# Kernel tuning notes

Hardware: AMD Instinct MI355X
Metric: run time of the kernel (lower is better)

The kernel has to match this reference:

```python
import jax, jax.numpy as jnp
import numpy as np

NUM_HEADS = 12


def setup_inputs() -> dict:
    key = jax.random.key(0)
    k0, k1, k2 = jax.random.split(key, 3)
    B, S, D = 2, 2048, 1536
    scale = 1.0 / np.sqrt(D)
    return {
        "hidden_states": jax.random.normal(k0, (B, S, D), dtype=jnp.float32),
        "W_fc": jax.random.normal(k1, (D, D), dtype=jnp.float32) * scale,
        "b_fc": jnp.zeros((D,), dtype=jnp.float32),
        "W_proj": jax.random.normal(k2, (D, D), dtype=jnp.float32) * scale,
        "b_proj": jnp.zeros((D,), dtype=jnp.float32),
    }


def reference(hidden_states, W_fc, b_fc, W_proj, b_proj):
    B, S, D = hidden_states.shape
    H = NUM_HEADS
    hd = D // H
    # value_states: [B, H, S, hd] (key_states == value_states in the original)
    v = (hidden_states @ W_fc.T + b_fc).reshape(B, S, H, hd).transpose(0, 2, 1, 3)
    # Uniform-weight causal sliding-window attention, window_h = 2^(h+1)-1.
    i = jnp.arange(S)[:, None]          # query pos
    j = jnp.arange(S)[None, :]          # key pos
    w = (2 ** jnp.arange(1, H + 1, dtype=jnp.int32) - 1)[:, None, None]  # [H,1,1]
    mask = (j <= i) & (j >= i - w + 1)                                    # [H,S,S]
    valid_len = jnp.minimum(i + 1, w).astype(v.dtype)                     # [H,S,1]
    attn = jnp.where(mask, 1.0 / valid_len, 0.0)                          # [H,S,S]
    # [H,S,S] x [B,H,S,hd] -> [B,S,H,hd] -> [B,S,D]
    out = jnp.einsum("hqk,bhkd->bqhd", attn, v).reshape(B, S, D)
    attn_weights = jnp.broadcast_to(attn[None], (B, H, S, S))
    return out @ W_proj.T + b_proj, attn_weights
```

## Files before the change

### kernel.cpp

```cpp
#include <hip/hip_runtime.h>
#include <hip/hip_bf16.h>

#define S_LEN   2048
#define DMODEL  1536
#define NBATCH  2
#define NHEADS  12
#define MROWS   (NBATCH * S_LEN)
#define NCHUNK  64
#define CHUNK   32

#define NGEMM_BLK  384
#define AW_BLK     3072
#define AW_TOTAL4  25165824u
#define AW_HALF4   12582912u

typedef unsigned short u16;
typedef __attribute__((ext_vector_type(8))) short bf16x8;
typedef __attribute__((ext_vector_type(4))) float f32x4;

__device__ __forceinline__ u16 f2bf(float x) {
  unsigned u = __float_as_uint(x);
  u += 0x7fffu + ((u >> 16) & 1u);
  return (u16)(u >> 16);
}
__device__ __forceinline__ float bf2f(u16 x) {
  return __uint_as_float(((unsigned)x) << 16);
}

#define N4_HID  1572864
#define N4_W    589824
__global__ void cvt_all(const float4* __restrict__ h, const float4* __restrict__ wf,
                        const float4* __restrict__ wp, ushort4* __restrict__ ho,
                        ushort4* __restrict__ wfo, ushort4* __restrict__ wpo) {
  int t = blockIdx.x * blockDim.x + threadIdx.x;
  const float4* src;
  ushort4* dst;
  int idx;
  if (t < N4_HID)            { src = h;  dst = ho;  idx = t; }
  else if (t < N4_HID + N4_W){ src = wf; dst = wfo; idx = t - N4_HID; }
  else                       { src = wp; dst = wpo; idx = t - N4_HID - N4_W; }
  float4 f = src[idx];
  ushort4 o;
  o.x = f2bf(f.x); o.y = f2bf(f.y); o.z = f2bf(f.z); o.w = f2bf(f.w);
  dst[idx] = o;
}

__device__ __forceinline__ void gld_lds16(u16* lds, const u16* g) {
  __builtin_amdgcn_global_load_lds(
      (const __attribute__((address_space(1))) unsigned int*)g,
      (__attribute__((address_space(3))) unsigned int*)lds, 16, 0, 0);
}

template <bool WITH_CSUM, typename CT>
__global__ __launch_bounds__(256)
void gemm_aw(const u16* __restrict__ A, const u16* __restrict__ B,
             const float* __restrict__ bias, CT* __restrict__ C,
             float* __restrict__ cs, f32x4* __restrict__ aw,
             unsigned aw0, unsigned awcnt, int Ndim, int Kdim) {
  if ((int)blockIdx.x >= NGEMM_BLK) {
    const unsigned stride = (gridDim.x - NGEMM_BLK) * 256u;
    const unsigned end = aw0 + awcnt;
    unsigned t = aw0 + (blockIdx.x - NGEMM_BLK) * 256u + threadIdx.x;
    for (; t < end; t += stride) {
      int j0 = (int)(t & 511u) << 2;
      int i  = (int)(t >> 9) & (S_LEN - 1);
      int bh = (int)(t >> 20);
      int h  = bh >= NHEADS ? bh - NHEADS : bh;
      int w  = (2 << h) - 1;
      int len = min(i + 1, w);
      float inv = 1.0f / (float)len;
      int lo = i - w + 1;
      f32x4 r;
      r.x = (j0     <= i && j0     >= lo) ? inv : 0.f;
      r.y = (j0 + 1 <= i && j0 + 1 >= lo) ? inv : 0.f;
      r.z = (j0 + 2 <= i && j0 + 2 >= lo) ? inv : 0.f;
      r.w = (j0 + 3 <= i && j0 + 3 >= lo) ? inv : 0.f;
      __builtin_nontemporal_store(r, &aw[t]);
    }
    return;
  }

  __shared__ __align__(16) u16 As[128 * 32];
  __shared__ __align__(16) u16 Bs[128 * 32];
  __shared__ float colpart[4][128];

  const int tid  = threadIdx.x;
  const int wave = tid >> 6;
  const int lane = tid & 63;
  const int l15  = lane & 15;
  const int quad = lane >> 4;
  const int bm = (blockIdx.x / (DMODEL / 128)) * 128;
  const int bn = (blockIdx.x % (DMODEL / 128)) * 128;
  const int wm = (wave >> 1) * 64;
  const int wn = (wave & 1) * 64;

  f32x4 acc[4][4] = {};

  const int srow = wave * 32 + (lane >> 2);
  const int skk  = (lane & 3) * 8;
  const u16* gA = A + (size_t)(bm + srow) * Kdim + skk;
  const u16* gB = B + (size_t)(bn + srow) * Kdim + skk;
  u16* lA = &As[(wave * 32) * 32];
  u16* lB = &Bs[(wave * 32) * 32];
  const size_t rstep16 = (size_t)16 * Kdim;

  for (int k0 = 0; k0 < Kdim; k0 += 32) {
    gld_lds16(lA,           gA + k0);
    gld_lds16(lA + 16 * 32, gA + k0 + rstep16);
    gld_lds16(lB,           gB + k0);
    gld_lds16(lB + 16 * 32, gB + k0 + rstep16);
    __syncthreads();

    bf16x8 af[4], bfr[4];
#pragma unroll
    for (int i = 0; i < 4; ++i)
      af[i] = *(const bf16x8*)&As[(wm + i * 16 + l15) * 32 + quad * 8];
#pragma unroll
    for (int j = 0; j < 4; ++j)
      bfr[j] = *(const bf16x8*)&Bs[(wn + j * 16 + l15) * 32 + quad * 8];
#pragma unroll
    for (int i = 0; i < 4; ++i)
#pragma unroll
      for (int j = 0; j < 4; ++j)
        acc[i][j] = __builtin_amdgcn_mfma_f32_16x16x32_bf16(af[i], bfr[j], acc[i][j], 0, 0, 0);
    __syncthreads();
  }

  const int r0 = quad * 4;
#pragma unroll
  for (int j = 0; j < 4; ++j) {
    const int col = bn + wn + j * 16 + l15;
    const float bj = bias[col];
    float sA = 0.f, sB = 0.f;
#pragma unroll
    for (int i = 0; i < 4; ++i) {
      const int row = bm + wm + i * 16 + r0;
#pragma unroll
      for (int r = 0; r < 4; ++r) {
        float cv = acc[i][j][r] + bj;
        if constexpr (sizeof(CT) == 2)
          C[(size_t)(row + r) * Ndim + col] = (CT)f2bf(cv);
        else
          C[(size_t)(row + r) * Ndim + col] = (CT)cv;
        if (WITH_CSUM) { if (i < 2) sA += cv; else sB += cv; }
      }
    }
    if (WITH_CSUM) {
      sA += __shfl_xor(sA, 16); sA += __shfl_xor(sA, 32);
      sB += __shfl_xor(sB, 16); sB += __shfl_xor(sB, 32);
      if (quad == 0) {
        colpart[(wm >> 5) | 0][wn + j * 16 + l15] = sA;
        colpart[(wm >> 5) | 1][wn + j * 16 + l15] = sB;
      }
    }
  }
  if (WITH_CSUM) {
    __syncthreads();
    if (tid < 128) {
      const int b  = bm >> 11;
      const int c0 = (bm & 2047) >> 5;
#pragma unroll
      for (int g = 0; g < 4; ++g)
        cs[((size_t)b * NCHUNK + c0 + g) * DMODEL + bn + tid] = colpart[g][tid];
    }
  }
}

__global__ void chunk_prefix(const float* __restrict__ cs, float* __restrict__ E) {
  int t = blockIdx.x * blockDim.x + threadIdx.x;
  int d = t % DMODEL;
  int c = (t / DMODEL) % NCHUNK;
  int b = t / (DMODEL * NCHUNK);
  const float* p = cs + (size_t)b * NCHUNK * DMODEL + d;
  float s = 0.f;
  for (int cc = 0; cc < c; ++cc) s += p[(size_t)cc * DMODEL];
  E[t] = s;
}

__global__ void winavg_strip(const u16* __restrict__ v, const float* __restrict__ E,
                             u16* __restrict__ A2) {
  int t = blockIdx.x * blockDim.x + threadIdx.x;
  int d = t % DMODEL;
  int s = (t / DMODEL) & 255;
  int b = t / (DMODEL * 256);
  const int h = d >> 7;
  const int w = (2 << h) - 1;
  const u16* vb  = v + (size_t)b * S_LEN * DMODEL + d;
  const float* Eb = E + (size_t)b * NCHUNK * DMODEL + d;

  const int i0 = s * 8;
  float lead = Eb[(size_t)(i0 >> 5) * DMODEL];
  for (int r = i0 & ~31; r < i0; ++r)
    lead += bf2f(vb[(size_t)r * DMODEL]);

  float trail = 0.f;
  if (i0 + 7 >= w) {
    const int jf = max(i0, w) - w;
    if (jf > 0) {
      const int ct = (jf - 1) >> 5;
      trail = Eb[(size_t)ct * DMODEL];
      for (int r = ct * 32; r < jf; ++r)
        trail += bf2f(vb[(size_t)r * DMODEL]);
    }
  }

  u16* out = A2 + ((size_t)(b * S_LEN + i0)) * DMODEL + d;
#pragma unroll
  for (int rr = 0; rr < 8; ++rr) {
    const int i = i0 + rr;
    lead += bf2f(vb[(size_t)i * DMODEL]);
    float o;
    if (i < w) {
      o = lead / (float)(i + 1);
    } else {
      trail += bf2f(vb[(size_t)(i - w) * DMODEL]);
      o = (lead - trail) / (float)w;
    }
    out[(size_t)rr * DMODEL] = f2bf(o);
  }
}

extern "C" void kernel_launch(void* const* d_in, const int* in_sizes, int n_in,
                              void* d_out, int out_size, void* d_ws, size_t ws_size,
                              hipStream_t stream) {
  const float* hidden = (const float*)d_in[0];
  const float* W_fc   = (const float*)d_in[1];
  const float* b_fc   = (const float*)d_in[2];
  const float* W_proj = (const float*)d_in[3];
  const float* b_proj = (const float*)d_in[4];
  float* outp = (float*)d_out;
  f32x4* aw = (f32x4*)(outp + (size_t)MROWS * DMODEL);

  char* ws = (char*)d_ws;
  u16*   A16   = (u16*)(ws);
  u16*   Wfc16 = (u16*)(ws + 12582912);
  u16*   Wpj16 = (u16*)(ws + 17301504);
  u16*   v16   = (u16*)(ws + 22020096);
  float* csums = (float*)(ws + 34603008);
  float* Epre  = (float*)(ws + 35389440);

  cvt_all<<<10752, 256, 0, stream>>>((const float4*)hidden, (const float4*)W_fc,
                                     (const float4*)W_proj, (ushort4*)A16,
                                     (ushort4*)Wfc16, (ushort4*)Wpj16);

  gemm_aw<true, u16><<<NGEMM_BLK + AW_BLK, 256, 0, stream>>>(
      A16, Wfc16, b_fc, v16, csums, aw, 0u, AW_HALF4, DMODEL, DMODEL);

  chunk_prefix<<<(NBATCH * NCHUNK * DMODEL) / 256, 256, 0, stream>>>(csums, Epre);

  winavg_strip<<<(NBATCH * (S_LEN / 8) * DMODEL) / 256, 256, 0, stream>>>(v16, Epre, A16);

  gemm_aw<false, float><<<NGEMM_BLK + AW_BLK, 256, 0, stream>>>(
      A16, Wpj16, b_proj, outp, nullptr, aw, AW_HALF4, AW_HALF4, DMODEL, DMODEL);
}
```

Baseline: 541.1 us.

## Fuse chunk prefix into window-average kernel and rebalance attn-weight writes across launches

Removes the separate chunk_prefix launch. The window-average kernel now computes its lead and trail prefix sums directly from the chunk sums with an in-register loop. Extra blocks are added to that kernel so it writes a slice of the attention-weight tensor, and the split of that output across the three launches is rebalanced. The final GEMM output is written with nontemporal stores. Each thread now does an O(chunks) loop, but one launch and one intermediate buffer round trip go away.

```diff
diff --git a/kernel.cpp b/kernel.cpp
--- a/kernel.cpp
+++ b/kernel.cpp
@@ -11,8 +11,12 @@
 
 #define NGEMM_BLK  384
 #define AW_BLK     3072
-#define AW_TOTAL4  25165824u
-#define AW_HALF4   12582912u
+#define WA_BLK     3072
+#define AW_BLK_W   512
+
+#define AW_TOT4    25165824u
+#define AW1_END    11324416u
+#define AWW_END    15098880u
 
 typedef unsigned short u16;
 typedef __attribute__((ext_vector_type(8))) short bf16x8;
@@ -25,6 +29,28 @@
 }
 __device__ __forceinline__ float bf2f(u16 x) {
   return __uint_as_float(((unsigned)x) << 16);
+}
+
+__device__ __forceinline__ void aw_write(f32x4* __restrict__ aw, unsigned aw0,
+                                         unsigned awcnt, unsigned bid,
+                                         unsigned nblk) {
+  const unsigned stride = nblk * 256u;
+  const unsigned end = aw0 + awcnt;
+  for (unsigned t = aw0 + bid * 256u + threadIdx.x; t < end; t += stride) {
+    int j0 = (int)(t & 511u) << 2;
+    int i  = (int)(t >> 9) & (S_LEN - 1);
+    int bh = (int)(t >> 20);
+    int h  = bh >= NHEADS ? bh - NHEADS : bh;
+    int w  = (2 << h) - 1;
+    float inv = 1.0f / (float)min(i + 1, w);
+    int lo = i - w + 1;
+    f32x4 r;
+    r.x = (j0     <= i && j0     >= lo) ? inv : 0.f;
+    r.y = (j0 + 1 <= i && j0 + 1 >= lo) ? inv : 0.f;
+    r.z = (j0 + 2 <= i && j0 + 2 >= lo) ? inv : 0.f;
+    r.w = (j0 + 3 <= i && j0 + 3 >= lo) ? inv : 0.f;
+    __builtin_nontemporal_store(r, &aw[t]);
+  }
 }
 
 #define N4_HID  1572864
@@ -58,25 +84,7 @@
              float* __restrict__ cs, f32x4* __restrict__ aw,
              unsigned aw0, unsigned awcnt, int Ndim, int Kdim) {
   if ((int)blockIdx.x >= NGEMM_BLK) {
-    const unsigned stride = (gridDim.x - NGEMM_BLK) * 256u;
-    const unsigned end = aw0 + awcnt;
-    unsigned t = aw0 + (blockIdx.x - NGEMM_BLK) * 256u + threadIdx.x;
-    for (; t < end; t += stride) {
-      int j0 = (int)(t & 511u) << 2;
-      int i  = (int)(t >> 9) & (S_LEN - 1);
-      int bh = (int)(t >> 20);
-      int h  = bh >= NHEADS ? bh - NHEADS : bh;
-      int w  = (2 << h) - 1;
-      int len = min(i + 1, w);
-      float inv = 1.0f / (float)len;
-      int lo = i - w + 1;
-      f32x4 r;
-      r.x = (j0     <= i && j0     >= lo) ? inv : 0.f;
-      r.y = (j0 + 1 <= i && j0 + 1 >= lo) ? inv : 0.f;
-      r.z = (j0 + 2 <= i && j0 + 2 >= lo) ? inv : 0.f;
-      r.w = (j0 + 3 <= i && j0 + 3 >= lo) ? inv : 0.f;
-      __builtin_nontemporal_store(r, &aw[t]);
-    }
+    aw_write(aw, aw0, awcnt, blockIdx.x - NGEMM_BLK, gridDim.x - NGEMM_BLK);
     return;
   }
 
@@ -141,7 +149,7 @@
         if constexpr (sizeof(CT) == 2)
           C[(size_t)(row + r) * Ndim + col] = (CT)f2bf(cv);
         else
-          C[(size_t)(row + r) * Ndim + col] = (CT)cv;
+          __builtin_nontemporal_store(cv, &C[(size_t)(row + r) * Ndim + col]);
         if (WITH_CSUM) { if (i < 2) sA += cv; else sB += cv; }
       }
     }
@@ -166,42 +174,44 @@
   }
 }
 
-__global__ void chunk_prefix(const float* __restrict__ cs, float* __restrict__ E) {
-  int t = blockIdx.x * blockDim.x + threadIdx.x;
-  int d = t % DMODEL;
-  int c = (t / DMODEL) % NCHUNK;
-  int b = t / (DMODEL * NCHUNK);
-  const float* p = cs + (size_t)b * NCHUNK * DMODEL + d;
-  float s = 0.f;
-  for (int cc = 0; cc < c; ++cc) s += p[(size_t)cc * DMODEL];
-  E[t] = s;
-}
-
-__global__ void winavg_strip(const u16* __restrict__ v, const float* __restrict__ E,
-                             u16* __restrict__ A2) {
+__global__ void winavg_aw(const u16* __restrict__ v, const float* __restrict__ cs,
+                          u16* __restrict__ A2, f32x4* __restrict__ aw,
+                          unsigned aw0, unsigned awcnt) {
+  if ((int)blockIdx.x >= WA_BLK) {
+    aw_write(aw, aw0, awcnt, blockIdx.x - WA_BLK, gridDim.x - WA_BLK);
+    return;
+  }
   int t = blockIdx.x * blockDim.x + threadIdx.x;
   int d = t % DMODEL;
   int s = (t / DMODEL) & 255;
   int b = t / (DMODEL * 256);
   const int h = d >> 7;
   const int w = (2 << h) - 1;
-  const u16* vb  = v + (size_t)b * S_LEN * DMODEL + d;
-  const float* Eb = E + (size_t)b * NCHUNK * DMODEL + d;
+  const u16* vb   = v  + (size_t)b * S_LEN * DMODEL + d;
+  const float* csb = cs + (size_t)b * NCHUNK * DMODEL + d;
 
   const int i0 = s * 8;
-  float lead = Eb[(size_t)(i0 >> 5) * DMODEL];
-  for (int r = i0 & ~31; r < i0; ++r)
+  const int c0 = i0 >> 5;
+  const bool need_trail = (i0 + 7 >= w);
+  const int jf = max(i0, w) - w;
+  const int ct = (need_trail && jf > 0) ? ((jf - 1) >> 5) : 0;
+
+  float E0 = 0.f, Et = 0.f;
+  for (int cc = 0; cc < c0; ++cc) {
+    float cv = csb[(size_t)cc * DMODEL];
+    E0 += cv;
+    if (cc < ct) Et += cv;
+  }
+
+  float lead = E0;
+  for (int r = c0 * 32; r < i0; ++r)
     lead += bf2f(vb[(size_t)r * DMODEL]);
 
   float trail = 0.f;
-  if (i0 + 7 >= w) {
-    const int jf = max(i0, w) - w;
-    if (jf > 0) {
-      const int ct = (jf - 1) >> 5;
-      trail = Eb[(size_t)ct * DMODEL];
-      for (int r = ct * 32; r < jf; ++r)
-        trail += bf2f(vb[(size_t)r * DMODEL]);
-    }
+  if (need_trail && jf > 0) {
+    trail = Et;
+    for (int r = ct * 32; r < jf; ++r)
+      trail += bf2f(vb[(size_t)r * DMODEL]);
   }
 
   u16* out = A2 + ((size_t)(b * S_LEN + i0)) * DMODEL + d;
@@ -237,19 +247,17 @@
   u16*   Wpj16 = (u16*)(ws + 17301504);
   u16*   v16   = (u16*)(ws + 22020096);
   float* csums = (float*)(ws + 34603008);
-  float* Epre  = (float*)(ws + 35389440);
 
   cvt_all<<<10752, 256, 0, stream>>>((const float4*)hidden, (const float4*)W_fc,
                                      (const float4*)W_proj, (ushort4*)A16,
                                      (ushort4*)Wfc16, (ushort4*)Wpj16);
 
   gemm_aw<true, u16><<<NGEMM_BLK + AW_BLK, 256, 0, stream>>>(
-      A16, Wfc16, b_fc, v16, csums, aw, 0u, AW_HALF4, DMODEL, DMODEL);
-
-  chunk_prefix<<<(NBATCH * NCHUNK * DMODEL) / 256, 256, 0, stream>>>(csums, Epre);
-
-  winavg_strip<<<(NBATCH * (S_LEN / 8) * DMODEL) / 256, 256, 0, stream>>>(v16, Epre, A16);
+      A16, Wfc16, b_fc, v16, csums, aw, 0u, AW1_END, DMODEL, DMODEL);
+
+  winavg_aw<<<WA_BLK + AW_BLK_W, 256, 0, stream>>>(
+      v16, csums, A16, aw, AW1_END, AWW_END - AW1_END);
 
   gemm_aw<false, float><<<NGEMM_BLK + AW_BLK, 256, 0, stream>>>(
-      A16, Wpj16, b_proj, outp, nullptr, aw, AW_HALF4, AW_HALF4, DMODEL, DMODEL);
-}
+      A16, Wpj16, b_proj, outp, nullptr, aw, AWW_END, AW_TOT4 - AWW_END, DMODEL, DMODEL);
+}
```

Measured after the change: 543.3 us. Within noise of the previous version (+0.4%).
